# Performance work log

Hardware: AMD Instinct MI355X
Metric: run time of the kernel (lower is better)

The kernel has to match this reference:

```python
import jax, jax.numpy as jnp
import numpy as np

DIM = 256
HEADS = 8
AGENT = 16
H = W = 64
B = 8


def _trunc_normal(key, shape, std=0.02):
    return jnp.clip(std * jax.random.normal(key, shape), -2 * std, 2 * std)


def setup_inputs() -> dict:
    key = jax.random.key(0)
    ks = jax.random.split(key, 16)
    c = DIM
    return {
        "input1": jax.random.normal(ks[0], (B, c, H, W), jnp.float32),
        "input2": jax.random.normal(ks[1], (B, c, H, W), jnp.float32),
        "guidmap": jax.random.normal(ks[2], (B, 1, H, W), jnp.float32),
        "kv_w": jax.random.normal(ks[3], (c, 2 * c), jnp.float32) * (c ** -0.5),
        "kv_b": jnp.zeros((2 * c,), jnp.float32),
        "q_w": jax.random.normal(ks[4], (1, c), jnp.float32),
        "q_b": jnp.zeros((c,), jnp.float32),
        "proj_w": jax.random.normal(ks[5], (c, c), jnp.float32) * (c ** -0.5),
        "proj_b": jnp.zeros((c,), jnp.float32),
        "dwc_w": jax.random.normal(ks[6], (c, 1, 3, 3), jnp.float32) * (1.0 / 3.0),
        "dwc_b": jnp.zeros((c,), jnp.float32),
        "an_bias": _trunc_normal(ks[7], (HEADS, AGENT, 4, 4)),
        "na_bias": _trunc_normal(ks[8], (HEADS, AGENT, 4, 4)),
        "ah_bias": _trunc_normal(ks[9], (1, HEADS, AGENT, H, 1)),
        "aw_bias": _trunc_normal(ks[10], (1, HEADS, AGENT, 1, W)),
        "ha_bias": _trunc_normal(ks[11], (1, HEADS, H, 1, AGENT)),
        "wa_bias": _trunc_normal(ks[12], (1, HEADS, 1, W, AGENT)),
    }


def _dwconv(v_img, dwc_w, dwc_b):
    # depthwise 3x3, padding 1 (groups = C)
    out = jax.lax.conv_general_dilated(
        v_img, dwc_w, window_strides=(1, 1), padding=((1, 1), (1, 1)),
        feature_group_count=v_img.shape[1],
        dimension_numbers=("NCHW", "OIHW", "NCHW"))
    return out + dwc_b[None, :, None, None]


def reference(input1, input2, guidmap, kv_w, kv_b, q_w, q_b, proj_w, proj_b,
              dwc_w, dwc_b, an_bias, na_bias, ah_bias, aw_bias, ha_bias, wa_bias):
    b, c, h, w = input1.shape
    n = h * w
    nh = an_bias.shape[0]
    A = an_bias.shape[1]
    hd = c // nh
    scale = hd ** -0.5
    ps = int(A ** 0.5)  # pool size (4)

    x1 = input1.reshape(b, c, n).transpose(0, 2, 1)   # (b,n,c)
    x2 = input2.reshape(b, c, n).transpose(0, 2, 1)
    g = guidmap.reshape(b, 1, n).transpose(0, 2, 1)   # (b,n,1)

    kv1 = x1 @ kv_w + kv_b
    k1, v1 = kv1[..., :c], kv1[..., c:]
    kv2 = x2 @ kv_w + kv_b
    k2, v2 = kv2[..., :c], kv2[..., c:]
    q = g @ q_w + q_b                                  # (b,n,c)

    # adaptive avg pool of q image to (ps, ps) -> agent tokens
    q_img = q.reshape(b, h, w, c)
    agent = q_img.reshape(b, ps, h // ps, ps, w // ps, c).mean(axis=(2, 4))  # (b,ps,ps,c)
    agent = agent.reshape(b, A, nh, hd).transpose(0, 2, 1, 3)                # (b,nh,A,hd)

    def heads(t):
        return t.reshape(b, n, nh, hd).transpose(0, 2, 1, 3)  # (b,nh,n,hd)

    qh, k1h, v1h, k2h, v2h = heads(q), heads(k1), heads(v1), heads(k2), heads(v2)

    # agent -> kv position bias: bilinear upsample (align_corners=False) + axial
    pb1 = jax.image.resize(an_bias, (nh, A, h, w), method="linear").reshape(1, nh, A, n)
    pb2 = (ah_bias + aw_bias).reshape(1, nh, A, n)
    pos_bias = pb1 + pb2

    attn1 = jax.nn.softmax((agent * scale) @ jnp.swapaxes(k1h, -2, -1) + pos_bias, axis=-1)
    agent_v1 = attn1 @ v1h                                    # (b,nh,A,hd)
    attn2 = jax.nn.softmax((agent * scale) @ jnp.swapaxes(k2h, -2, -1) + pos_bias, axis=-1)
    agent_v2 = attn2 @ v2h

    # query -> agent bias
    ab1 = jax.image.resize(na_bias, (nh, A, h, w), method="linear").reshape(1, nh, A, n)
    ab1 = ab1.transpose(0, 1, 3, 2)                           # (1,nh,n,A)
    ab2 = (ha_bias + wa_bias).reshape(1, nh, n, A)
    agent_bias = ab1 + ab2

    q_attn = jax.nn.softmax((qh * scale) @ jnp.swapaxes(agent, -2, -1) + agent_bias, axis=-1)
    out1 = (q_attn @ agent_v1).transpose(0, 2, 1, 3).reshape(b, n, c)
    out2 = (q_attn @ agent_v2).transpose(0, 2, 1, 3).reshape(b, n, c)

    v1_img = v1.reshape(b, h, w, c).transpose(0, 3, 1, 2)
    v2_img = v2.reshape(b, h, w, c).transpose(0, 3, 1, 2)
    out1 = out1 + _dwconv(v1_img, dwc_w, dwc_b).reshape(b, c, n).transpose(0, 2, 1)
    out2 = out2 + _dwconv(v2_img, dwc_w, dwc_b).reshape(b, c, n).transpose(0, 2, 1)

    out1 = out1 @ proj_w + proj_b
    out2 = out2 @ proj_w + proj_b
    o1 = out1.transpose(0, 2, 1).reshape(b, c, h, w) + input1
    o2 = out2.transpose(0, 2, 1).reshape(b, c, h, w) + input2
    return (o1, o2)
```

## Files before the change

### kernel.cpp

```cpp
#include <hip/hip_runtime.h>
#include <hip/hip_bf16.h>
#include <cstddef>

#define B_   8
#define C_   256
#define HH   64
#define WW   64
#define NPOS 4096
#define NH   8
#define HD   32
#define NA   16
#define NHA  128
#define SCALE 0.17677669529663687f

typedef unsigned short u16;
typedef __attribute__((ext_vector_type(8))) short bf16x8;
typedef __attribute__((ext_vector_type(4))) float f32x4;

__device__ __forceinline__ float bfbits2f(u16 u) {
  union { unsigned int i; float f; } x; x.i = ((unsigned int)u) << 16; return x.f;
}
__device__ __forceinline__ u16 f2bfbits(float f) {
  union { float f; unsigned int i; } x; x.f = f;
  unsigned int r = x.i + 0x7fffu + ((x.i >> 16) & 1u);
  return (u16)(r >> 16);
}
__device__ __forceinline__ void unpack8(const uint4 v, float* f) {
  f[0] = bfbits2f((u16)(v.x & 0xffff)); f[1] = bfbits2f((u16)(v.x >> 16));
  f[2] = bfbits2f((u16)(v.y & 0xffff)); f[3] = bfbits2f((u16)(v.y >> 16));
  f[4] = bfbits2f((u16)(v.z & 0xffff)); f[5] = bfbits2f((u16)(v.z >> 16));
  f[6] = bfbits2f((u16)(v.w & 0xffff)); f[7] = bfbits2f((u16)(v.w >> 16));
}

__global__ __launch_bounds__(256) void k_agent(const float* __restrict__ g,
                                               const float* __restrict__ q_w,
                                               const float* __restrict__ q_b,
                                               float* __restrict__ agent_buf) {
  const int b = blockIdx.x;
  const int t = threadIdx.x;
  __shared__ float red[256];
  __shared__ float gb[16];
  const int ag = t >> 4, sub = t & 15;
  const int p1 = ag >> 2, p2 = ag & 3;
  const int y = p1 * 16 + sub, x0 = p2 * 16;
  const float* gp = g + (size_t)b * NPOS + y * WW + x0;
  float s = 0.f;
#pragma unroll
  for (int i = 0; i < 16; ++i) s += gp[i];
  red[t] = s;
  __syncthreads();
  if (sub == 0) {
    float tot = 0.f;
    for (int i = 0; i < 16; ++i) tot += red[(ag << 4) + i];
    gb[ag] = tot * (1.0f / 256.0f);
  }
  __syncthreads();
  for (int idx = t; idx < NA * C_; idx += 256) {
    const int a = idx >> 8, ci = idx & 255;
    const int h = ci >> 5, d = ci & 31;
    agent_buf[(((size_t)b * NH + h) * NA + a) * HD + d] = gb[a] * q_w[ci] + q_b[ci];
  }
}

__global__ __launch_bounds__(256) void k_wtilde(const u16* __restrict__ Wkt, const float* __restrict__ kv_b,
                                                const float* __restrict__ agent_buf,
                                                u16* __restrict__ wt, float* __restrict__ kvbD) {
  const int h = blockIdx.x, b = blockIdx.y;
  const int t = threadIdx.x;
  __shared__ u16 Wk[32 * 256];
  __shared__ float ags[16][32];
#pragma unroll
  for (int i = 0; i < 4; ++i) {
    const int idx = t + 256 * i;
    const int r = idx >> 5, sl = idx & 31;
    *(uint4*)(Wk + r * 256 + sl * 8) = *(const uint4*)(Wkt + (size_t)(h * 32 + r) * C_ + sl * 8);
  }
#pragma unroll
  for (int i = 0; i < 2; ++i) {
    const int idx = t + 256 * i;
    const int a = idx >> 5, d = idx & 31;
    ags[a][d] = agent_buf[(((size_t)b * NH + h) * NA + a) * HD + d] * SCALE;
  }
  __syncthreads();
  const int a = t >> 4, cb = (t & 15) * 16;
  float o[16];
#pragma unroll
  for (int k = 0; k < 16; ++k) o[k] = 0.f;
  for (int d = 0; d < 32; ++d) {
    const float av = ags[a][d];
#pragma unroll
    for (int k = 0; k < 16; ++k) o[k] += av * bfbits2f(Wk[d * 256 + cb + k]);
  }
  unsigned int w[8];
#pragma unroll
  for (int q = 0; q < 8; ++q)
    w[q] = (unsigned int)f2bfbits(o[2 * q]) | ((unsigned int)f2bfbits(o[2 * q + 1]) << 16);
  u16* op = wt + ((size_t)(b * NHA + h * 16 + a)) * C_ + cb;
  *(uint4*)op = make_uint4(w[0], w[1], w[2], w[3]);
  *(uint4*)(op + 8) = make_uint4(w[4], w[5], w[6], w[7]);
  if ((t & 15) == 0) {
    float s = 0.f;
#pragma unroll
    for (int d = 0; d < 32; ++d) s += ags[a][d] * kv_b[h * 32 + d];
    kvbD[b * NHA + h * 16 + a] = s;
  }
}

__global__ __launch_bounds__(256) void k_bias(const float* __restrict__ an_b,
                                              const float* __restrict__ ah_b, const float* __restrict__ aw_b,
                                              float* __restrict__ posbT) {
  const int idx = blockIdx.x * 256 + threadIdx.x;
  const int ha = idx & 127;
  const int pos = idx >> 7;
  const int h = ha >> 4, a = ha & 15;
  const int y = pos >> 6, x = pos & 63;
  const float sy = (y + 0.5f) * 0.0625f - 0.5f;
  const float sx = (x + 0.5f) * 0.0625f - 0.5f;
  const int y0 = (int)floorf(sy);
  const int x0 = (int)floorf(sx);
  const float wy = sy - (float)y0, wx = sx - (float)x0;
  const int y0c = min(max(y0, 0), 3), y1c = min(max(y0 + 1, 0), 3);
  const int x0c = min(max(x0, 0), 3), x1c = min(max(x0 + 1, 0), 3);
  const float* an4 = an_b + ((size_t)h * NA + a) * 16;
  const float pa_ = (1.f - wy) * ((1.f - wx) * an4[y0c * 4 + x0c] + wx * an4[y0c * 4 + x1c]) +
                    wy * ((1.f - wx) * an4[y1c * 4 + x0c] + wx * an4[y1c * 4 + x1c]);
  posbT[(size_t)pos * NHA + ha] = pa_ + ah_b[((size_t)h * NA + a) * HH + y] + aw_b[((size_t)h * NA + a) * WW + x];
}

__global__ __launch_bounds__(256) void k_prep_in(const float* __restrict__ in1, const float* __restrict__ in2,
                                                 u16* __restrict__ At1, u16* __restrict__ At2) {
  const int z = blockIdx.z;
  const int src = z >> 3, b = z & 7;
  const float* in = src ? in2 : in1;
  u16* At = src ? At2 : At1;
  const int pos0 = blockIdx.x * 64;
  const int ci0 = blockIdx.y * 64;
  __shared__ float tile[64][68];
  const int t = threadIdx.x;
  const int rpos = (t & 15) << 2, rci = t >> 4;
#pragma unroll
  for (int i = 0; i < 4; ++i) {
    const int ci_l = rci + 16 * i;
    const float4 v = *(const float4*)(in + ((size_t)b * C_ + ci0 + ci_l) * NPOS + pos0 + rpos);
    tile[ci_l][rpos + 0] = v.x; tile[ci_l][rpos + 1] = v.y;
    tile[ci_l][rpos + 2] = v.z; tile[ci_l][rpos + 3] = v.w;
  }
  __syncthreads();
#pragma unroll
  for (int i = 0; i < 2; ++i) {
    const int u = t + 256 * i;
    const int p = u >> 3, s = u & 7;
    unsigned int w[4];
#pragma unroll
    for (int q = 0; q < 4; ++q) {
      const u16 lo = f2bfbits(tile[s * 8 + 2 * q][p]);
      const u16 hi = f2bfbits(tile[s * 8 + 2 * q + 1][p]);
      w[q] = (unsigned int)lo | ((unsigned int)hi << 16);
    }
    *(uint4*)(At + ((size_t)(pos0 + p)) * C_ + (size_t)b * NPOS * C_ + ci0 + s * 8) =
        make_uint4(w[0], w[1], w[2], w[3]);
  }
}

__global__ __launch_bounds__(256) void k_prep_w(const float* __restrict__ kv_w, const float* __restrict__ proj_w,
                                                u16* __restrict__ Wkt, u16* __restrict__ Pwt) {
  const int x = blockIdx.x;
  const float* W; u16* T; int j0, ci0, ncols;
  if (x < 32) { W = kv_w;  T = Wkt; j0 = (x & 7) * 64; ci0 = (x >> 3) * 64; ncols = 512; }
  else        { W = proj_w; T = Pwt; j0 = ((x - 32) & 3) * 64; ci0 = ((x - 32) >> 2) * 64; ncols = 256; }
  __shared__ float tile[64][68];
  const int t = threadIdx.x;
  const int rj = (t & 15) << 2, rci = t >> 4;
#pragma unroll
  for (int i = 0; i < 4; ++i) {
    const int ci_l = rci + 16 * i;
    const float4 v = *(const float4*)(W + (size_t)(ci0 + ci_l) * ncols + j0 + rj);
    tile[ci_l][rj + 0] = v.x; tile[ci_l][rj + 1] = v.y;
    tile[ci_l][rj + 2] = v.z; tile[ci_l][rj + 3] = v.w;
  }
  __syncthreads();
#pragma unroll
  for (int i = 0; i < 2; ++i) {
    const int u = t + 256 * i;
    const int p = u >> 3, s = u & 7;
    unsigned int w[4];
#pragma unroll
    for (int q = 0; q < 4; ++q) {
      const u16 lo = f2bfbits(tile[s * 8 + 2 * q][p]);
      const u16 hi = f2bfbits(tile[s * 8 + 2 * q + 1][p]);
      w[q] = (unsigned int)lo | ((unsigned int)hi << 16);
    }
    *(uint4*)(T + (size_t)(j0 + p) * C_ + ci0 + s * 8) = make_uint4(w[0], w[1], w[2], w[3]);
  }
}

__global__ __launch_bounds__(256) void k_prep_dwc(const float* __restrict__ dwc_w, const float* __restrict__ dwc_b,
                                                  float* __restrict__ dwcT) {
  const int ci = threadIdx.x;
#pragma unroll
  for (int q = 0; q < 9; ++q) dwcT[q * 256 + ci] = dwc_w[ci * 9 + q];
  dwcT[9 * 256 + ci] = dwc_b[ci];
}

__global__ __launch_bounds__(256) void k_v_mfma(const u16* __restrict__ At1, const u16* __restrict__ At2,
                                                const u16* __restrict__ Wkt, const float* __restrict__ kv_b,
                                                u16* __restrict__ v1, u16* __restrict__ v2) {
  const int z = blockIdx.z;
  const int src = z >> 3, b = z & 7;
  const u16* At = src ? At2 : At1;
  u16* vout = src ? v2 : v1;
  const int pos0 = blockIdx.x * 128;
  const int j0 = blockIdx.y * 128;

  __shared__ __align__(16) u16 SM[16384];
  u16* Ab = SM;
  u16* Bb = SM + 8192;

  const int t = threadIdx.x;
  const int wave = t >> 6, lane = t & 63;
  const int wm = wave >> 1, wn = wave & 1;
  const int g = lane >> 4;

  const u16* Ag = Wkt + (size_t)(256 + j0) * C_;
  const u16* Bg = At + ((size_t)b * NPOS + pos0) * C_;

  f32x4 acc[4][4];
#pragma unroll
  for (int m = 0; m < 4; ++m)
#pragma unroll
    for (int n = 0; n < 4; ++n) { acc[m][n][0]=0.f; acc[m][n][1]=0.f; acc[m][n][2]=0.f; acc[m][n][3]=0.f; }

  uint4 ra[4], rb[4];
#define V_LOAD(KT)                                                         \
  _Pragma("unroll") for (int i = 0; i < 4; ++i) {                          \
    const int u = t + 256 * i, rr = u >> 3, ss = u & 7;                    \
    ra[i] = *(const uint4*)(Ag + (size_t)rr * C_ + (KT) * 64 + ss * 8);    \
    rb[i] = *(const uint4*)(Bg + (size_t)rr * C_ + (KT) * 64 + ss * 8);    \
  }
#define V_WRITE()                                                          \
  _Pragma("unroll") for (int i = 0; i < 4; ++i) {                          \
    const int u = t + 256 * i, rr = u >> 3, ss = u & 7;                    \
    const int sw = ((ss ^ (rr & 7)) << 3);                                 \
    *(uint4*)(Ab + rr * 64 + sw) = ra[i];                                  \
    *(uint4*)(Bb + rr * 64 + sw) = rb[i];                                  \
  }

  V_LOAD(0);
  V_WRITE();
  V_LOAD(1);
  __syncthreads();

  for (int kt = 0; kt < 4; ++kt) {
#pragma unroll
    for (int kk = 0; kk < 2; ++kk) {
      bf16x8 af[4], bfr[4];
#pragma unroll
      for (int m = 0; m < 4; ++m) {
        const int r = wm * 64 + m * 16 + (lane & 15);
        af[m] = *(const bf16x8*)(Ab + r * 64 + (((kk * 4 + g) ^ (r & 7)) << 3));
      }
#pragma unroll
      for (int n = 0; n < 4; ++n) {
        const int c = wn * 64 + n * 16 + (lane & 15);
        bfr[n] = *(const bf16x8*)(Bb + c * 64 + (((kk * 4 + g) ^ (c & 7)) << 3));
      }
#pragma unroll
      for (int m = 0; m < 4; ++m)
#pragma unroll
        for (int n = 0; n < 4; ++n)
          acc[m][n] = __builtin_amdgcn_mfma_f32_16x16x32_bf16(af[m], bfr[n], acc[m][n], 0, 0, 0);
    }
    if (kt < 3) {
      __syncthreads();
      V_WRITE();
      if (kt < 2) V_LOAD(kt + 2);
      __syncthreads();
    }
  }
#undef V_LOAD
#undef V_WRITE

  __syncthreads();
#pragma unroll
  for (int m = 0; m < 4; ++m) {
    const int jl = wm * 64 + m * 16 + (lane >> 4) * 4;
    const float4 bv = *(const float4*)(kv_b + 256 + j0 + jl);
#pragma unroll
    for (int n = 0; n < 4; ++n) {
      const int pos_l = wn * 64 + n * 16 + (lane & 15);
      const f32x4 a = acc[m][n];
      ushort4 st;
      st.x = f2bfbits(a[0] + bv.x); st.y = f2bfbits(a[1] + bv.y);
      st.z = f2bfbits(a[2] + bv.z); st.w = f2bfbits(a[3] + bv.w);
      const int slot = (jl >> 3) ^ (pos_l & 7);
      *(ushort4*)(SM + pos_l * 128 + slot * 8 + (jl & 7)) = st;
    }
  }
  __syncthreads();
#pragma unroll
  for (int i = 0; i < 8; ++i) {
    const int idx = t + 256 * i;
    const int row = idx >> 4, sl = idx & 15;
    const uint4 v = *(const uint4*)(SM + row * 128 + ((sl ^ (row & 7)) << 3));
    *(uint4*)(vout + ((size_t)b * NPOS + pos0 + row) * C_ + j0 + sl * 8) = v;
  }
}

__global__ __launch_bounds__(256) void k_score(const u16* __restrict__ At1, const u16* __restrict__ At2,
                                               const u16* __restrict__ wt, const float* __restrict__ posbT,
                                               const float* __restrict__ kvbD,
                                               u16* __restrict__ E, float* __restrict__ lsumP) {
  const int z = blockIdx.z;
  const int src = z >> 3, b = z & 7;
  const int sb = src * 8 + b;
  const u16* At = src ? At2 : At1;
  const int pos0 = blockIdx.x * 128;

  __shared__ __align__(16) u16 SM[16384];
  __shared__ float lsum_sm[2][128];
  u16* Ab = SM;
  u16* Bb = SM + 8192;

  const int t = threadIdx.x;
  const int wave = t >> 6, lane = t & 63;
  const int wm = wave >> 1, wn = wave & 1;
  const int g = lane >> 4;

  const u16* Ag = At + ((size_t)b * NPOS + pos0) * C_;
  const u16* Bg = wt + (size_t)b * NHA * C_;

  f32x4 acc[4][4];
#pragma unroll
  for (int m = 0; m < 4; ++m)
#pragma unroll
    for (int n = 0; n < 4; ++n) { acc[m][n][0]=0.f; acc[m][n][1]=0.f; acc[m][n][2]=0.f; acc[m][n][3]=0.f; }

  uint4 ra[4], rb[4];
#define S_LOAD(KT)                                                         \
  _Pragma("unroll") for (int i = 0; i < 4; ++i) {                          \
    const int u = t + 256 * i, rr = u >> 3, ss = u & 7;                    \
    ra[i] = *(const uint4*)(Ag + (size_t)rr * C_ + (KT) * 64 + ss * 8);    \
    rb[i] = *(const uint4*)(Bg + (size_t)rr * C_ + (KT) * 64 + ss * 8);    \
  }
#define S_WRITE()                                                          \
  _Pragma("unroll") for (int i = 0; i < 4; ++i) {                          \
    const int u = t + 256 * i, rr = u >> 3, ss = u & 7;                    \
    const int sw = ((ss ^ (rr & 7)) << 3);                                 \
    *(uint4*)(Ab + rr * 64 + sw) = ra[i];                                  \
    *(uint4*)(Bb + rr * 64 + sw) = rb[i];                                  \
  }

  S_LOAD(0);
  S_WRITE();
  S_LOAD(1);
  __syncthreads();

  for (int kt = 0; kt < 4; ++kt) {
#pragma unroll
    for (int kk = 0; kk < 2; ++kk) {
      bf16x8 af[4], bfr[4];
#pragma unroll
      for (int m = 0; m < 4; ++m) {
        const int r = wm * 64 + m * 16 + (lane & 15);
        af[m] = *(const bf16x8*)(Ab + r * 64 + (((kk * 4 + g) ^ (r & 7)) << 3));
      }
#pragma unroll
      for (int n = 0; n < 4; ++n) {
        const int c = wn * 64 + n * 16 + (lane & 15);
        bfr[n] = *(const bf16x8*)(Bb + c * 64 + (((kk * 4 + g) ^ (c & 7)) << 3));
      }
#pragma unroll
      for (int m = 0; m < 4; ++m)
#pragma unroll
        for (int n = 0; n < 4; ++n)
          acc[m][n] = __builtin_amdgcn_mfma_f32_16x16x32_bf16(af[m], bfr[n], acc[m][n], 0, 0, 0);
    }
    if (kt < 3) {
      __syncthreads();
      S_WRITE();
      if (kt < 2) S_LOAD(kt + 2);
      __syncthreads();
    }
  }
#undef S_LOAD
#undef S_WRITE

  __syncthreads();
  float ls[4] = {0.f, 0.f, 0.f, 0.f};
#pragma unroll
  for (int n = 0; n < 4; ++n) {
    const int ha_l = wn * 64 + n * 16 + (lane & 15);
    const float kb = kvbD[b * NHA + ha_l];
#pragma unroll
    for (int m = 0; m < 4; ++m) {
      const int pos_l = wm * 64 + m * 16 + (lane >> 4) * 4;
      float e[4];
#pragma unroll
      for (int j = 0; j < 4; ++j) {
        const float s = acc[m][n][j] + posbT[(size_t)(pos0 + pos_l + j) * NHA + ha_l] + kb;
        e[j] = __expf(s);
        ls[n] += e[j];
      }
      ushort4 st;
      st.x = f2bfbits(e[0]); st.y = f2bfbits(e[1]); st.z = f2bfbits(e[2]); st.w = f2bfbits(e[3]);
      const int sw = (pos_l >> 3) ^ (ha_l & 15);
      *(ushort4*)(SM + ha_l * 128 + sw * 8 + (pos_l & 7)) = st;
    }
  }
#pragma unroll
  for (int n = 0; n < 4; ++n) {
    float v = ls[n];
    v += __shfl_xor(v, 16);
    v += __shfl_xor(v, 32);
    ls[n] = v;
  }
  if (lane < 16) {
#pragma unroll
    for (int n = 0; n < 4; ++n) lsum_sm[wm][wn * 64 + n * 16 + lane] = ls[n];
  }
  __syncthreads();
  if (t < 128)
    lsumP[((size_t)sb * 32 + blockIdx.x) * NHA + t] = lsum_sm[0][t] + lsum_sm[1][t];
#pragma unroll
  for (int i = 0; i < 8; ++i) {
    const int idx = t + 256 * i;
    const int row = idx >> 4, sl = idx & 15;
    const uint4 v = *(const uint4*)(SM + row * 128 + ((sl ^ (row & 15)) << 3));
    *(uint4*)(E + ((size_t)sb * NHA + row) * NPOS + pos0 + sl * 8) = v;
  }
}

__global__ __launch_bounds__(256) void k_pv(const float* __restrict__ in1, const float* __restrict__ in2,
                                            const u16* __restrict__ E, float* __restrict__ T_p) {
  const int kc = blockIdx.x;
  const int ci0 = blockIdx.y * 128;
  const int sb = blockIdx.z;
  const int src = sb >> 3, b = sb & 7;
  const float* in = src ? in2 : in1;
  const int kpos0 = kc * 512;

  __shared__ __align__(16) u16 As[8192];
  __shared__ __align__(16) u16 Bs[8192];

  const int t = threadIdx.x;
  const int wave = t >> 6, lane = t & 63;
  const int wm = wave >> 1, wn = wave & 1;
  const int g = lane >> 4;

  const float* Ain = in + (size_t)b * C_ * NPOS;
  const u16* Eg = E + (size_t)sb * NHA * NPOS;

  f32x4 acc[4][4];
#pragma unroll
  for (int m = 0; m < 4; ++m)
#pragma unroll
    for (int n = 0; n < 4; ++n) { acc[m][n][0]=0.f; acc[m][n][1]=0.f; acc[m][n][2]=0.f; acc[m][n][3]=0.f; }

  float4 pa[8];
  uint4 pb[4];
#define PV_LOAD(KT)                                                            \
  _Pragma("unroll") for (int i = 0; i < 8; ++i) {                              \
    const int idx = t + 256 * i, rr = idx >> 4, fq = idx & 15;                 \
    pa[i] = *(const float4*)(Ain + (size_t)(ci0 + rr) * NPOS + kpos0 + (KT) * 64 + fq * 4); \
  }                                                                            \
  _Pragma("unroll") for (int i = 0; i < 4; ++i) {                              \
    const int idx = t + 256 * i, rr = idx >> 3, ss = idx & 7;                  \
    pb[i] = *(const uint4*)(Eg + (size_t)rr * NPOS + kpos0 + (KT) * 64 + ss * 8); \
  }
#define PV_WRITE()                                                             \
  _Pragma("unroll") for (int i = 0; i < 8; ++i) {                              \
    const int idx = t + 256 * i, rr = idx >> 4, fq = idx & 15;                 \
    ushort4 st;                                                                \
    st.x = f2bfbits(pa[i].x); st.y = f2bfbits(pa[i].y);                        \
    st.z = f2bfbits(pa[i].z); st.w = f2bfbits(pa[i].w);                        \
    const int sw = ((fq >> 1) ^ (rr & 7));                                     \
    *(ushort4*)(As + rr * 64 + sw * 8 + (fq & 1) * 4) = st;                    \
  }                                                                            \
  _Pragma("unroll") for (int i = 0; i < 4; ++i) {                              \
    const int idx = t + 256 * i, rr = idx >> 3, ss = idx & 7;                  \
    *(uint4*)(Bs + rr * 64 + ((ss ^ (rr & 7)) << 3)) = pb[i];                  \
  }

  PV_LOAD(0);
  PV_WRITE();
  PV_LOAD(1);
  __syncthreads();

  for (int kt = 0; kt < 8; ++kt) {
#pragma unroll
    for (int kk = 0; kk < 2; ++kk) {
      bf16x8 af[4], bfr[4];
#pragma unroll
      for (int m = 0; m < 4; ++m) {
        const int r = wm * 64 + m * 16 + (lane & 15);
        af[m] = *(const bf16x8*)(As + r * 64 + (((kk * 4 + g) ^ (r & 7)) << 3));
      }
#pragma unroll
      for (int n = 0; n < 4; ++n) {
        const int c = wn * 64 + n * 16 + (lane & 15);
        bfr[n] = *(const bf16x8*)(Bs + c * 64 + (((kk * 4 + g) ^ (c & 7)) << 3));
      }
#pragma unroll
      for (int m = 0; m < 4; ++m)
#pragma unroll
        for (int n = 0; n < 4; ++n)
          acc[m][n] = __builtin_amdgcn_mfma_f32_16x16x32_bf16(af[m], bfr[n], acc[m][n], 0, 0, 0);
    }
    if (kt < 7) {
      __syncthreads();
      PV_WRITE();
      if (kt < 6) PV_LOAD(kt + 2);
      __syncthreads();
    }
  }
#undef PV_LOAD
#undef PV_WRITE

#pragma unroll
  for (int m = 0; m < 4; ++m) {
    const int ci_l = wm * 64 + m * 16 + (lane >> 4) * 4;
#pragma unroll
    for (int n = 0; n < 4; ++n) {
      const int ha_l = wn * 64 + n * 16 + (lane & 15);
      const f32x4 a = acc[m][n];
      *(float4*)(T_p + (((size_t)sb * 8 + kc) * NHA + ha_l) * C_ + ci0 + ci_l) =
          make_float4(a[0], a[1], a[2], a[3]);
    }
  }
}

__global__ __launch_bounds__(256) void k_agentv(const float* __restrict__ T_p, const float* __restrict__ lsumP,
                                                const u16* __restrict__ Wkt, const float* __restrict__ kv_b,
                                                float* __restrict__ agent_v) {
  const int h = blockIdx.x, sb = blockIdx.y;
  const int t = threadIdx.x;
  __shared__ float Tred[16 * 256];
  __shared__ u16 Wv[32 * 256];
  __shared__ float lsum_s[16];
#pragma unroll
  for (int i = 0; i < 4; ++i) {
    const int idx = t + 256 * i;
    const int r = idx >> 5, sl = idx & 31;
    *(uint4*)(Wv + r * 256 + sl * 8) = *(const uint4*)(Wkt + (size_t)(256 + h * 32 + r) * C_ + sl * 8);
  }
#pragma unroll
  for (int i = 0; i < 16; ++i) {
    const int idx = t + 256 * i;
    const int a = idx >> 8, ci = idx & 255;
    float s = 0.f;
#pragma unroll
    for (int kc = 0; kc < 8; ++kc)
      s += T_p[(((size_t)sb * 8 + kc) * NHA + h * 16 + a) * C_ + ci];
    Tred[a * 256 + ci] = s;
  }
  if (t < 16) {
    float s = 0.f;
#pragma unroll
    for (int pt = 0; pt < 32; ++pt) s += lsumP[((size_t)sb * 32 + pt) * NHA + h * 16 + t];
    lsum_s[t] = s;
  }
  __syncthreads();
  const int a = t >> 4, dp = (t & 15) * 2;
  float o0 = 0.f, o1 = 0.f;
  const float* Tr = Tred + a * 256;
  for (int ci = 0; ci < 256; ++ci) {
    const float tv = Tr[ci];
    o0 += tv * bfbits2f(Wv[dp * 256 + ci]);
    o1 += tv * bfbits2f(Wv[(dp + 1) * 256 + ci]);
  }
  const float inv = 1.0f / lsum_s[a];
  float* op = agent_v + (size_t)sb * NHA * HD + (h * 16 + a) * HD + dp;
  op[0] = o0 * inv + kv_b[256 + h * 32 + dp];
  op[1] = o1 * inv + kv_b[256 + h * 32 + dp + 1];
}

__global__ __launch_bounds__(256) void k_qattn(const float* __restrict__ g,
                                               const float* __restrict__ q_w, const float* __restrict__ q_b,
                                               const float* __restrict__ agent_buf,
                                               const float* __restrict__ agent_v,
                                               const float* __restrict__ na_b,
                                               const float* __restrict__ ha_b,
                                               const float* __restrict__ wa_b,
                                               u16* __restrict__ o1s, u16* __restrict__ o2s) {
  const int h = blockIdx.y;
  const int sb = blockIdx.z;
  const int src = sb >> 3, b = sb & 7;
  u16* out = src ? o2s : o1s;
  const int t = threadIdx.x;
  const int pos = blockIdx.x * 256 + t;
  __shared__ float dotW[16], dotB[16];
  __shared__ float av[16][32];
  __shared__ float nab[16][16];
  for (int idx = t; idx < 512; idx += 256) {
    const int a = idx >> 5, d = idx & 31;
    av[a][d] = agent_v[(size_t)sb * NHA * HD + (h * 16 + a) * HD + d];
  }
  if (t < 256 && t < 16 * 16) {
    const int a = t >> 4, q = t & 15;
    nab[a][q] = na_b[((size_t)h * NA + a) * 16 + q];
  }
  if (t < 16) {
    float dw = 0.f, db = 0.f;
    const float* agp = agent_buf + (((size_t)b * NH + h) * NA + t) * HD;
#pragma unroll
    for (int d = 0; d < HD; ++d) {
      const float ad = agp[d];
      dw += ad * q_w[h * HD + d];
      db += ad * q_b[h * HD + d];
    }
    dotW[t] = dw * SCALE;
    dotB[t] = db * SCALE;
  }
  __syncthreads();
  const int y = pos >> 6, x = pos & 63;
  const float sy = (y + 0.5f) * 0.0625f - 0.5f;
  const float sx = (x + 0.5f) * 0.0625f - 0.5f;
  const int y0 = (int)floorf(sy);
  const int x0 = (int)floorf(sx);
  const float wy = sy - (float)y0, wx = sx - (float)x0;
  const int y0c = min(max(y0, 0), 3), y1c = min(max(y0 + 1, 0), 3);
  const int x0c = min(max(x0, 0), 3), x1c = min(max(x0 + 1, 0), 3);
  const float c00 = (1.f - wy) * (1.f - wx), c01 = (1.f - wy) * wx;
  const float c10 = wy * (1.f - wx), c11 = wy * wx;
  const int i00 = y0c * 4 + x0c, i01 = y0c * 4 + x1c;
  const int i10 = y1c * 4 + x0c, i11 = y1c * 4 + x1c;
  const float* hp = ha_b + ((size_t)h * HH + y) * NA;
  const float* wp = wa_b + ((size_t)h * WW + x) * NA;
  const float gv = g[(size_t)b * NPOS + pos];
  float s[16];
  float m = -1e30f;
#pragma unroll
  for (int a = 0; a < 16; ++a) {
    const float nv = c00 * nab[a][i00] + c01 * nab[a][i01] + c10 * nab[a][i10] + c11 * nab[a][i11];
    s[a] = gv * dotW[a] + dotB[a] + nv + hp[a] + wp[a];
    m = fmaxf(m, s[a]);
  }
  float l = 0.f;
#pragma unroll
  for (int a = 0; a < 16; ++a) {
    s[a] = __expf(s[a] - m);
    l += s[a];
  }
  const float inv = 1.0f / l;
  float o[32] = {};
#pragma unroll
  for (int a = 0; a < 16; ++a) {
    const float pa = s[a] * inv;
#pragma unroll
    for (int q = 0; q < 8; ++q) {
      const float4 v4 = *(const float4*)&av[a][q * 4];
      o[q * 4 + 0] += pa * v4.x; o[q * 4 + 1] += pa * v4.y;
      o[q * 4 + 2] += pa * v4.z; o[q * 4 + 3] += pa * v4.w;
    }
  }
  u16* op = out + ((size_t)b * NPOS + pos) * C_ + h * HD;
#pragma unroll
  for (int blk = 0; blk < 4; ++blk) {
    unsigned int w1[4];
#pragma unroll
    for (int q = 0; q < 4; ++q)
      w1[q] = (unsigned int)f2bfbits(o[blk * 8 + 2 * q]) | ((unsigned int)f2bfbits(o[blk * 8 + 2 * q + 1]) << 16);
    *(uint4*)(op + blk * 8) = make_uint4(w1[0], w1[1], w1[2], w1[3]);
  }
}

__global__ __launch_bounds__(256) void k_dwconv(const u16* __restrict__ v1, const u16* __restrict__ v2,
                                                const float* __restrict__ dwcT,
                                                u16* __restrict__ o1s, u16* __restrict__ o2s) {
  const u16* V = blockIdx.z ? v2 : v1;
  u16* out = blockIdx.z ? o2s : o1s;
  const int b = blockIdx.y;
  const int t = threadIdx.x;
  const int cg = t & 31;
  const int ch = cg * 8;
  const int px = t >> 5;
  const int pos = (blockIdx.x << 3) + px;
  const int y = pos >> 6, x = pos & 63;

  float acc[8];
  {
    const float4 b0 = *(const float4*)(dwcT + 9 * 256 + ch);
    const float4 b1 = *(const float4*)(dwcT + 9 * 256 + ch + 4);
    acc[0] = b0.x; acc[1] = b0.y; acc[2] = b0.z; acc[3] = b0.w;
    acc[4] = b1.x; acc[5] = b1.y; acc[6] = b1.z; acc[7] = b1.w;
  }
  const u16* vb = V + (size_t)b * NPOS * C_ + ch;
#pragma unroll
  for (int dy = -1; dy <= 1; ++dy) {
    const int yy = y + dy;
    if (yy < 0 || yy > 63) continue;
#pragma unroll
    for (int dx = -1; dx <= 1; ++dx) {
      const int xx = x + dx;
      if (xx < 0 || xx > 63) continue;
      const int q = (dy + 1) * 3 + (dx + 1);
      const float4 w0 = *(const float4*)(dwcT + q * 256 + ch);
      const float4 w1 = *(const float4*)(dwcT + q * 256 + ch + 4);
      const uint4 vv = *(const uint4*)(vb + (size_t)(yy * 64 + xx) * C_);
      float f8[8];
      unpack8(vv, f8);
      acc[0] += w0.x * f8[0]; acc[1] += w0.y * f8[1];
      acc[2] += w0.z * f8[2]; acc[3] += w0.w * f8[3];
      acc[4] += w1.x * f8[4]; acc[5] += w1.y * f8[5];
      acc[6] += w1.z * f8[6]; acc[7] += w1.w * f8[7];
    }
  }
  u16* op = out + ((size_t)b * NPOS + pos) * C_ + ch;
  const uint4 ov = *(const uint4*)op;
  float f8[8];
  unpack8(ov, f8);
  unsigned int wo[4];
#pragma unroll
  for (int q2 = 0; q2 < 4; ++q2)
    wo[q2] = (unsigned int)f2bfbits(f8[2 * q2] + acc[2 * q2]) |
             ((unsigned int)f2bfbits(f8[2 * q2 + 1] + acc[2 * q2 + 1]) << 16);
  *(uint4*)op = make_uint4(wo[0], wo[1], wo[2], wo[3]);
}

__global__ __launch_bounds__(256) void k_proj_mfma(const u16* __restrict__ o1s, const u16* __restrict__ o2s,
                                                   const u16* __restrict__ Pwt, const float* __restrict__ proj_b,
                                                   const float* __restrict__ in1, const float* __restrict__ in2,
                                                   float* __restrict__ out1, float* __restrict__ out2) {
  const int z = blockIdx.z;
  const int src = z >> 3, b = z & 7;
  const u16* S = src ? o2s : o1s;
  const float* inp = src ? in2 : in1;
  float* outp = src ? out2 : out1;
  const int pos0 = blockIdx.x * 128;
  const int co0 = blockIdx.y * 128;

  __shared__ __align__(16) u16 SM[16384];
  u16* Ab = SM;
  u16* Bb = SM + 8192;
  float* SMF = (float*)SM;

  const int t = threadIdx.x;
  const int wave = t >> 6, lane = t & 63;
  const int wm = wave >> 1, wn = wave & 1;
  const int g = lane >> 4;

  const u16* Ag = S + ((size_t)b * NPOS + pos0) * C_;
  const u16* Bg = Pwt + (size_t)co0 * C_;

  f32x4 acc[4][4];
#pragma unroll
  for (int m = 0; m < 4; ++m)
#pragma unroll
    for (int n = 0; n < 4; ++n) { acc[m][n][0]=0.f; acc[m][n][1]=0.f; acc[m][n][2]=0.f; acc[m][n][3]=0.f; }

  uint4 ra[4], rb[4];
#define PJ_LOAD(KT)                                                        \
  _Pragma("unroll") for (int i = 0; i < 4; ++i) {                          \
    const int u = t + 256 * i, rr = u >> 3, ss = u & 7;                    \
    ra[i] = *(const uint4*)(Ag + (size_t)rr * C_ + (KT) * 64 + ss * 8);    \
    rb[i] = *(const uint4*)(Bg + (size_t)rr * C_ + (KT) * 64 + ss * 8);    \
  }
#define PJ_WRITE()                                                         \
  _Pragma("unroll") for (int i = 0; i < 4; ++i) {                          \
    const int u = t + 256 * i, rr = u >> 3, ss = u & 7;                    \
    const int sw = ((ss ^ (rr & 7)) << 3);                                 \
    *(uint4*)(Ab + rr * 64 + sw) = ra[i];                                  \
    *(uint4*)(Bb + rr * 64 + sw) = rb[i];                                  \
  }

  PJ_LOAD(0);
  PJ_WRITE();
  PJ_LOAD(1);
  __syncthreads();

  for (int kt = 0; kt < 4; ++kt) {
#pragma unroll
    for (int kk = 0; kk < 2; ++kk) {
      bf16x8 af[4], bfr[4];
#pragma unroll
      for (int m = 0; m < 4; ++m) {
        const int r = wm * 64 + m * 16 + (lane & 15);
        af[m] = *(const bf16x8*)(Ab + r * 64 + (((kk * 4 + g) ^ (r & 7)) << 3));
      }
#pragma unroll
      for (int n = 0; n < 4; ++n) {
        const int c = wn * 64 + n * 16 + (lane & 15);
        bfr[n] = *(const bf16x8*)(Bb + c * 64 + (((kk * 4 + g) ^ (c & 7)) << 3));
      }
#pragma unroll
      for (int m = 0; m < 4; ++m)
#pragma unroll
        for (int n = 0; n < 4; ++n)
          acc[m][n] = __builtin_amdgcn_mfma_f32_16x16x32_bf16(af[m], bfr[n], acc[m][n], 0, 0, 0);
    }
    if (kt < 3) {
      __syncthreads();
      PJ_WRITE();
      if (kt < 2) PJ_LOAD(kt + 2);
      __syncthreads();
    }
  }
#undef PJ_LOAD
#undef PJ_WRITE

#pragma unroll
  for (int hf = 0; hf < 2; ++hf) {
    __syncthreads();
    if (wn == hf) {
#pragma unroll
      for (int n = 0; n < 4; ++n) {
        const int co_l = n * 16 + (lane & 15);
#pragma unroll
        for (int m = 0; m < 4; ++m) {
          const int pos_l = wm * 64 + m * 16 + (lane >> 4) * 4;
          const int slot = (pos_l >> 2) ^ (co_l & 7);
          const f32x4 a = acc[m][n];
          *(float4*)(SMF + co_l * 128 + slot * 4) = make_float4(a[0], a[1], a[2], a[3]);
        }
      }
    }
    __syncthreads();
#pragma unroll
    for (int i = 0; i < 8; ++i) {
      const int idx = t + 256 * i;
      const int row = idx >> 5, sl = idx & 31;
      const float4 v = *(const float4*)(SMF + row * 128 + ((sl ^ (row & 7)) << 2));
      const int co = co0 + hf * 64 + row;
      const float pb = proj_b[co];
      const size_t base = ((size_t)b * C_ + co) * NPOS + pos0 + sl * 4;
      const float4 res = *(const float4*)(inp + base);
      *(float4*)(outp + base) = make_float4(v.x + pb + res.x, v.y + pb + res.y,
                                            v.z + pb + res.z, v.w + pb + res.w);
    }
  }
}

extern "C" void kernel_launch(void* const* d_in, const int* in_sizes, int n_in,
                              void* d_out, int out_size, void* d_ws, size_t ws_size,
                              hipStream_t stream) {
  const float* input1 = (const float*)d_in[0];
  const float* input2 = (const float*)d_in[1];
  const float* guid   = (const float*)d_in[2];
  const float* kv_w   = (const float*)d_in[3];
  const float* kv_b   = (const float*)d_in[4];
  const float* q_w    = (const float*)d_in[5];
  const float* q_b    = (const float*)d_in[6];
  const float* proj_w = (const float*)d_in[7];
  const float* proj_b = (const float*)d_in[8];
  const float* dwc_w  = (const float*)d_in[9];
  const float* dwc_b  = (const float*)d_in[10];
  const float* an_b   = (const float*)d_in[11];
  const float* na_b   = (const float*)d_in[12];
  const float* ah_b   = (const float*)d_in[13];
  const float* aw_b   = (const float*)d_in[14];
  const float* ha_b   = (const float*)d_in[15];
  const float* wa_b   = (const float*)d_in[16];

  char* W = (char*)d_ws;
  u16* At1 = (u16*)W;        W += (size_t)B_ * NPOS * C_ * 2;
  u16* At2 = (u16*)W;        W += (size_t)B_ * NPOS * C_ * 2;
  u16* v1  = (u16*)W;        W += (size_t)B_ * NPOS * C_ * 2;
  u16* v2  = (u16*)W;        W += (size_t)B_ * NPOS * C_ * 2;
  u16* o1s = (u16*)W;        W += (size_t)B_ * NPOS * C_ * 2;
  u16* o2s = (u16*)W;        W += (size_t)B_ * NPOS * C_ * 2;
  u16* E   = (u16*)W;        W += (size_t)16 * NHA * NPOS * 2;
  float* T_p = (float*)W;    W += (size_t)16 * 8 * NHA * C_ * 4;
  u16* Wkt = (u16*)W;        W += (size_t)512 * C_ * 2;
  u16* Pwt = (u16*)W;        W += (size_t)C_ * C_ * 2;
  u16* wt  = (u16*)W;        W += (size_t)B_ * NHA * C_ * 2;
  float* posbT = (float*)W;  W += (size_t)NPOS * NHA * 4;
  float* agentb = (float*)W; W += (size_t)B_ * NH * NA * HD * 4;
  float* kvbD   = (float*)W; W += (size_t)B_ * NHA * 4;
  float* lsumP  = (float*)W; W += (size_t)16 * 32 * NHA * 4;
  float* agent_v = (float*)W; W += (size_t)16 * NHA * HD * 4;
  float* dwcT    = (float*)W; W += (size_t)10 * 256 * 4;

  float* out1 = (float*)d_out;
  float* out2 = out1 + (size_t)B_ * C_ * NPOS;

  hipLaunchKernelGGL(k_agent, dim3(B_), dim3(256), 0, stream, guid, q_w, q_b, agentb);
  hipLaunchKernelGGL(k_bias, dim3((NHA * NPOS) / 256), dim3(256), 0, stream,
                     an_b, ah_b, aw_b, posbT);
  hipLaunchKernelGGL(k_prep_w, dim3(48), dim3(256), 0, stream, kv_w, proj_w, Wkt, Pwt);
  hipLaunchKernelGGL(k_prep_dwc, dim3(1), dim3(256), 0, stream, dwc_w, dwc_b, dwcT);
  hipLaunchKernelGGL(k_wtilde, dim3(NH, B_), dim3(256), 0, stream, Wkt, kv_b, agentb, wt, kvbD);
  hipLaunchKernelGGL(k_prep_in, dim3(64, 4, 16), dim3(256), 0, stream, input1, input2, At1, At2);
  hipLaunchKernelGGL(k_v_mfma, dim3(32, 2, 16), dim3(256), 0, stream,
                     At1, At2, Wkt, kv_b, v1, v2);
  hipLaunchKernelGGL(k_score, dim3(32, 1, 16), dim3(256), 0, stream,
                     At1, At2, wt, posbT, kvbD, E, lsumP);
  hipLaunchKernelGGL(k_pv, dim3(8, 2, 16), dim3(256), 0, stream, input1, input2, E, T_p);
  hipLaunchKernelGGL(k_agentv, dim3(NH, 16), dim3(256), 0, stream, T_p, lsumP, Wkt, kv_b, agent_v);
  hipLaunchKernelGGL(k_qattn, dim3(NPOS / 256, NH, 16), dim3(256), 0, stream,
                     guid, q_w, q_b, agentb, agent_v, na_b, ha_b, wa_b, o1s, o2s);
  hipLaunchKernelGGL(k_dwconv, dim3(NPOS / 8, B_, 2), dim3(256), 0, stream,
                     v1, v2, dwcT, o1s, o2s);
  hipLaunchKernelGGL(k_proj_mfma, dim3(32, 2, 16), dim3(256), 0, stream,
                     o1s, o2s, Pwt, proj_b, input1, input2, out1, out2);
}
```

Before: 246.0 us.

## Fuse query-agent attention with depthwise conv into one kernel

Merges the query-to-agent softmax/aggregation kernel and the depthwise 3x3 conv kernel into a single kernel. Each thread now owns 8 channels of one position and adds the attention output straight into the conv accumulator. This drops a full bf16 write and read-back of the o1s/o2s intermediates and one launch. The per-agent query dot products (agent·q_w, agent·q_b) move into k_wtilde and are stored in a small buffer. In exchange, each block stages agent_v and na_bias into shared memory, and the 16-way softmax is recomputed by the four threads that share a head.

```diff
diff --git a/kernel.cpp b/kernel.cpp
--- a/kernel.cpp
+++ b/kernel.cpp
@@ -64,7 +64,9 @@
 
 __global__ __launch_bounds__(256) void k_wtilde(const u16* __restrict__ Wkt, const float* __restrict__ kv_b,
                                                 const float* __restrict__ agent_buf,
-                                                u16* __restrict__ wt, float* __restrict__ kvbD) {
+                                                const float* __restrict__ q_w, const float* __restrict__ q_b,
+                                                u16* __restrict__ wt, float* __restrict__ kvbD,
+                                                float* __restrict__ qd) {
   const int h = blockIdx.x, b = blockIdx.y;
   const int t = threadIdx.x;
   __shared__ u16 Wk[32 * 256];
@@ -103,6 +105,16 @@
 #pragma unroll
     for (int d = 0; d < 32; ++d) s += ags[a][d] * kv_b[h * 32 + d];
     kvbD[b * NHA + h * 16 + a] = s;
+  }
+  if ((t & 15) == 1) {
+    float s1 = 0.f, s2 = 0.f;
+#pragma unroll
+    for (int d = 0; d < 32; ++d) {
+      s1 += ags[a][d] * q_w[h * HD + d];
+      s2 += ags[a][d] * q_b[h * HD + d];
+    }
+    qd[(size_t)b * 256 + h * 32 + a * 2 + 0] = s1;
+    qd[(size_t)b * 256 + h * 32 + a * 2 + 1] = s2;
   }
 }
 
@@ -574,45 +586,74 @@
   op[1] = o1 * inv + kv_b[256 + h * 32 + dp + 1];
 }
 
-__global__ __launch_bounds__(256) void k_qattn(const float* __restrict__ g,
-                                               const float* __restrict__ q_w, const float* __restrict__ q_b,
-                                               const float* __restrict__ agent_buf,
-                                               const float* __restrict__ agent_v,
-                                               const float* __restrict__ na_b,
-                                               const float* __restrict__ ha_b,
-                                               const float* __restrict__ wa_b,
-                                               u16* __restrict__ o1s, u16* __restrict__ o2s) {
-  const int h = blockIdx.y;
-  const int sb = blockIdx.z;
-  const int src = sb >> 3, b = sb & 7;
+__global__ __launch_bounds__(256) void k_odw(const u16* __restrict__ v1, const u16* __restrict__ v2,
+                                             const float* __restrict__ dwcT,
+                                             const float* __restrict__ g,
+                                             const float* __restrict__ qd,
+                                             const float* __restrict__ agent_v,
+                                             const float* __restrict__ na_b,
+                                             const float* __restrict__ ha_b,
+                                             const float* __restrict__ wa_b,
+                                             u16* __restrict__ o1s, u16* __restrict__ o2s) {
+  const int src = blockIdx.z;
+  const int b = blockIdx.y;
+  const int sb = src * 8 + b;
+  const u16* V = src ? v2 : v1;
   u16* out = src ? o2s : o1s;
   const int t = threadIdx.x;
-  const int pos = blockIdx.x * 256 + t;
-  __shared__ float dotW[16], dotB[16];
-  __shared__ float av[16][32];
-  __shared__ float nab[16][16];
-  for (int idx = t; idx < 512; idx += 256) {
-    const int a = idx >> 5, d = idx & 31;
-    av[a][d] = agent_v[(size_t)sb * NHA * HD + (h * 16 + a) * HD + d];
-  }
-  if (t < 256 && t < 16 * 16) {
-    const int a = t >> 4, q = t & 15;
-    nab[a][q] = na_b[((size_t)h * NA + a) * 16 + q];
-  }
-  if (t < 16) {
-    float dw = 0.f, db = 0.f;
-    const float* agp = agent_buf + (((size_t)b * NH + h) * NA + t) * HD;
-#pragma unroll
-    for (int d = 0; d < HD; ++d) {
-      const float ad = agp[d];
-      dw += ad * q_w[h * HD + d];
-      db += ad * q_b[h * HD + d];
-    }
-    dotW[t] = dw * SCALE;
-    dotB[t] = db * SCALE;
-  }
-  __syncthreads();
+  const int cg = t & 31;
+  const int ch = cg * 8;
+  const int px = t >> 5;
+  const int pos = (blockIdx.x << 3) + px;
   const int y = pos >> 6, x = pos & 63;
+  const int h = cg >> 2;
+  const int dsl = (cg & 3) * 8;
+
+  __shared__ float av_s[128][32];
+  __shared__ float nab[8][16][16];
+  __shared__ float qds[8][16][2];
+#pragma unroll
+  for (int i = 0; i < 16; ++i) {
+    const int idx = t + 256 * i;
+    ((float*)av_s)[idx] = agent_v[(size_t)sb * NHA * HD + idx];
+  }
+#pragma unroll
+  for (int i = 0; i < 8; ++i) {
+    const int idx = t + 256 * i;
+    ((float*)nab)[idx] = na_b[idx];
+  }
+  ((float*)qds)[t] = qd[(size_t)b * 256 + t];
+  __syncthreads();
+
+  float acc[8];
+  {
+    const float4 b0 = *(const float4*)(dwcT + 9 * 256 + ch);
+    const float4 b1 = *(const float4*)(dwcT + 9 * 256 + ch + 4);
+    acc[0] = b0.x; acc[1] = b0.y; acc[2] = b0.z; acc[3] = b0.w;
+    acc[4] = b1.x; acc[5] = b1.y; acc[6] = b1.z; acc[7] = b1.w;
+  }
+  const u16* vb = V + (size_t)b * NPOS * C_ + ch;
+#pragma unroll
+  for (int dy = -1; dy <= 1; ++dy) {
+    const int yy = y + dy;
+    if (yy < 0 || yy > 63) continue;
+#pragma unroll
+    for (int dx = -1; dx <= 1; ++dx) {
+      const int xx = x + dx;
+      if (xx < 0 || xx > 63) continue;
+      const int q = (dy + 1) * 3 + (dx + 1);
+      const float4 w0 = *(const float4*)(dwcT + q * 256 + ch);
+      const float4 w1 = *(const float4*)(dwcT + q * 256 + ch + 4);
+      const uint4 vv = *(const uint4*)(vb + (size_t)(yy * 64 + xx) * C_);
+      float f8[8];
+      unpack8(vv, f8);
+      acc[0] += w0.x * f8[0]; acc[1] += w0.y * f8[1];
+      acc[2] += w0.z * f8[2]; acc[3] += w0.w * f8[3];
+      acc[4] += w1.x * f8[4]; acc[5] += w1.y * f8[5];
+      acc[6] += w1.z * f8[6]; acc[7] += w1.w * f8[7];
+    }
+  }
+
   const float sy = (y + 0.5f) * 0.0625f - 0.5f;
   const float sx = (x + 0.5f) * 0.0625f - 0.5f;
   const int y0 = (int)floorf(sy);
@@ -631,8 +672,9 @@
   float m = -1e30f;
 #pragma unroll
   for (int a = 0; a < 16; ++a) {
-    const float nv = c00 * nab[a][i00] + c01 * nab[a][i01] + c10 * nab[a][i10] + c11 * nab[a][i11];
-    s[a] = gv * dotW[a] + dotB[a] + nv + hp[a] + wp[a];
+    const float nv = c00 * nab[h][a][i00] + c01 * nab[h][a][i01] +
+                     c10 * nab[h][a][i10] + c11 * nab[h][a][i11];
+    s[a] = gv * qds[h][a][0] + qds[h][a][1] + nv + hp[a] + wp[a];
     m = fmaxf(m, s[a]);
   }
   float l = 0.f;
@@ -642,78 +684,21 @@
     l += s[a];
   }
   const float inv = 1.0f / l;
-  float o[32] = {};
 #pragma unroll
   for (int a = 0; a < 16; ++a) {
     const float pa = s[a] * inv;
-#pragma unroll
-    for (int q = 0; q < 8; ++q) {
-      const float4 v4 = *(const float4*)&av[a][q * 4];
-      o[q * 4 + 0] += pa * v4.x; o[q * 4 + 1] += pa * v4.y;
-      o[q * 4 + 2] += pa * v4.z; o[q * 4 + 3] += pa * v4.w;
-    }
-  }
-  u16* op = out + ((size_t)b * NPOS + pos) * C_ + h * HD;
-#pragma unroll
-  for (int blk = 0; blk < 4; ++blk) {
-    unsigned int w1[4];
-#pragma unroll
-    for (int q = 0; q < 4; ++q)
-      w1[q] = (unsigned int)f2bfbits(o[blk * 8 + 2 * q]) | ((unsigned int)f2bfbits(o[blk * 8 + 2 * q + 1]) << 16);
-    *(uint4*)(op + blk * 8) = make_uint4(w1[0], w1[1], w1[2], w1[3]);
-  }
-}
-
-__global__ __launch_bounds__(256) void k_dwconv(const u16* __restrict__ v1, const u16* __restrict__ v2,
-                                                const float* __restrict__ dwcT,
-                                                u16* __restrict__ o1s, u16* __restrict__ o2s) {
-  const u16* V = blockIdx.z ? v2 : v1;
-  u16* out = blockIdx.z ? o2s : o1s;
-  const int b = blockIdx.y;
-  const int t = threadIdx.x;
-  const int cg = t & 31;
-  const int ch = cg * 8;
-  const int px = t >> 5;
-  const int pos = (blockIdx.x << 3) + px;
-  const int y = pos >> 6, x = pos & 63;
-
-  float acc[8];
-  {
-    const float4 b0 = *(const float4*)(dwcT + 9 * 256 + ch);
-    const float4 b1 = *(const float4*)(dwcT + 9 * 256 + ch + 4);
-    acc[0] = b0.x; acc[1] = b0.y; acc[2] = b0.z; acc[3] = b0.w;
-    acc[4] = b1.x; acc[5] = b1.y; acc[6] = b1.z; acc[7] = b1.w;
-  }
-  const u16* vb = V + (size_t)b * NPOS * C_ + ch;
-#pragma unroll
-  for (int dy = -1; dy <= 1; ++dy) {
-    const int yy = y + dy;
-    if (yy < 0 || yy > 63) continue;
-#pragma unroll
-    for (int dx = -1; dx <= 1; ++dx) {
-      const int xx = x + dx;
-      if (xx < 0 || xx > 63) continue;
-      const int q = (dy + 1) * 3 + (dx + 1);
-      const float4 w0 = *(const float4*)(dwcT + q * 256 + ch);
-      const float4 w1 = *(const float4*)(dwcT + q * 256 + ch + 4);
-      const uint4 vv = *(const uint4*)(vb + (size_t)(yy * 64 + xx) * C_);
-      float f8[8];
-      unpack8(vv, f8);
-      acc[0] += w0.x * f8[0]; acc[1] += w0.y * f8[1];
-      acc[2] += w0.z * f8[2]; acc[3] += w0.w * f8[3];
-      acc[4] += w1.x * f8[4]; acc[5] += w1.y * f8[5];
-      acc[6] += w1.z * f8[6]; acc[7] += w1.w * f8[7];
-    }
-  }
+    const float4 v0 = *(const float4*)&av_s[h * 16 + a][dsl];
+    const float4 v1q = *(const float4*)&av_s[h * 16 + a][dsl + 4];
+    acc[0] += pa * v0.x; acc[1] += pa * v0.y; acc[2] += pa * v0.z; acc[3] += pa * v0.w;
+    acc[4] += pa * v1q.x; acc[5] += pa * v1q.y; acc[6] += pa * v1q.z; acc[7] += pa * v1q.w;
+  }
+
   u16* op = out + ((size_t)b * NPOS + pos) * C_ + ch;
-  const uint4 ov = *(const uint4*)op;
-  float f8[8];
-  unpack8(ov, f8);
   unsigned int wo[4];
 #pragma unroll
   for (int q2 = 0; q2 < 4; ++q2)
-    wo[q2] = (unsigned int)f2bfbits(f8[2 * q2] + acc[2 * q2]) |
-             ((unsigned int)f2bfbits(f8[2 * q2 + 1] + acc[2 * q2 + 1]) << 16);
+    wo[q2] = (unsigned int)f2bfbits(acc[2 * q2]) |
+             ((unsigned int)f2bfbits(acc[2 * q2 + 1]) << 16);
   *(uint4*)op = make_uint4(wo[0], wo[1], wo[2], wo[3]);
 }
 
@@ -869,6 +854,7 @@
   float* lsumP  = (float*)W; W += (size_t)16 * 32 * NHA * 4;
   float* agent_v = (float*)W; W += (size_t)16 * NHA * HD * 4;
   float* dwcT    = (float*)W; W += (size_t)10 * 256 * 4;
+  float* qd      = (float*)W; W += (size_t)B_ * NHA * 2 * 4;
 
   float* out1 = (float*)d_out;
   float* out2 = out1 + (size_t)B_ * C_ * NPOS;
@@ -878,7 +864,8 @@
                      an_b, ah_b, aw_b, posbT);
   hipLaunchKernelGGL(k_prep_w, dim3(48), dim3(256), 0, stream, kv_w, proj_w, Wkt, Pwt);
   hipLaunchKernelGGL(k_prep_dwc, dim3(1), dim3(256), 0, stream, dwc_w, dwc_b, dwcT);
-  hipLaunchKernelGGL(k_wtilde, dim3(NH, B_), dim3(256), 0, stream, Wkt, kv_b, agentb, wt, kvbD);
+  hipLaunchKernelGGL(k_wtilde, dim3(NH, B_), dim3(256), 0, stream,
+                     Wkt, kv_b, agentb, q_w, q_b, wt, kvbD, qd);
   hipLaunchKernelGGL(k_prep_in, dim3(64, 4, 16), dim3(256), 0, stream, input1, input2, At1, At2);
   hipLaunchKernelGGL(k_v_mfma, dim3(32, 2, 16), dim3(256), 0, stream,
                      At1, At2, Wkt, kv_b, v1, v2);
@@ -886,10 +873,8 @@
                      At1, At2, wt, posbT, kvbD, E, lsumP);
   hipLaunchKernelGGL(k_pv, dim3(8, 2, 16), dim3(256), 0, stream, input1, input2, E, T_p);
   hipLaunchKernelGGL(k_agentv, dim3(NH, 16), dim3(256), 0, stream, T_p, lsumP, Wkt, kv_b, agent_v);
-  hipLaunchKernelGGL(k_qattn, dim3(NPOS / 256, NH, 16), dim3(256), 0, stream,
-                     guid, q_w, q_b, agentb, agent_v, na_b, ha_b, wa_b, o1s, o2s);
-  hipLaunchKernelGGL(k_dwconv, dim3(NPOS / 8, B_, 2), dim3(256), 0, stream,
-                     v1, v2, dwcT, o1s, o2s);
+  hipLaunchKernelGGL(k_odw, dim3(NPOS / 8, B_, 2), dim3(256), 0, stream,
+                     v1, v2, dwcT, guid, qd, agent_v, na_b, ha_b, wa_b, o1s, o2s);
   hipLaunchKernelGGL(k_proj_mfma, dim3(32, 2, 16), dim3(256), 0, stream,
                      o1s, o2s, Pwt, proj_b, input1, input2, out1, out2);
 }
```

Measured after the change: 302.5 us. 1.23x slower.
